# Performance work log

Measured on AMD Instinct MI355X. Metric: run time of the kernel, lower is better.

The kernel has to match this reference:

```python
import jax, jax.numpy as jnp
import numpy as np

B, S, V, K = 8, 128, 32000, 32


def setup_inputs() -> dict:
    key = jax.random.key(0)
    ks = jax.random.split(key, 8)
    return {
        "neural_logit": jax.random.normal(ks[0], (B, S, V), dtype=jnp.float32),
        "optor_vals": jax.random.randint(ks[1], (B, S, K), 0, V),
        "optor_dists": jax.random.uniform(ks[2], (B, S, K), dtype=jnp.float32) * 100.0,
        "const_vals": jax.random.randint(ks[3], (B, S, K), 0, V),
        "const_dists": jax.random.uniform(ks[4], (B, S, K), dtype=jnp.float32) * 100.0,
        "prev_words": jax.random.randint(ks[5], (B, S), 0, V),
        "optor_lamda": jnp.array([0.7], dtype=jnp.float32),
        "const_lamda": jnp.array([0.7], dtype=jnp.float32),
        "optor_temp": jnp.array([10.0], dtype=jnp.float32),
        "const_temp": jnp.array([10.0], dtype=jnp.float32),
    }


def _knn_prob(vals, dists, temp, vocab):
    # kernel-density: softmax over negative distances, scatter-add into vocab ids
    b, s, k = vals.shape
    w = jax.nn.softmax(-dists / temp, axis=-1)            # [B,S,K]
    rows = jnp.arange(b * s)[:, None]                     # [BS,1]
    p = jnp.zeros((b * s, vocab), w.dtype)
    p = p.at[rows, vals.reshape(b * s, k)].add(w.reshape(b * s, k))
    return p.reshape(b, s, vocab)


def reference(neural_logit, optor_vals, optor_dists, const_vals, const_dists,
              prev_words, optor_lamda, const_lamda, optor_temp, const_temp):
    nmt_prob = jax.nn.softmax(neural_logit, axis=-1)      # [B,S,V]

    optor_knn = _knn_prob(optor_vals, optor_dists, optor_temp[0], V)
    optor_combined = optor_lamda[0] * optor_knn + (1.0 - optor_lamda[0]) * nmt_prob

    const_knn = _knn_prob(const_vals, const_dists, const_temp[0], V)
    const_combined = const_lamda[0] * const_knn + (1.0 - const_lamda[0]) * nmt_prob

    pw = prev_words                                        # [B,S]
    optor_mask = (pw <= 88) | ((pw >= 91) & (pw <= 291))
    const_mask = (pw == 89) | (pw == 90) | (pw >= 292)

    combined = (optor_combined * optor_mask[:, :, None].astype(nmt_prob.dtype)
                + const_combined * const_mask[:, :, None].astype(nmt_prob.dtype))
    return combined
```

## Files before the change

### kernel.cpp

```cpp
#include <hip/hip_runtime.h>
#include <math.h>

constexpr int Bc = 8, Sc = 128, Vc = 32000, Kc = 32;
constexpr int ROWS = Bc * Sc;
constexpr int V4 = Vc / 4;
constexpr int NTA = 256;
constexpr int NTB = 256;
constexpr int CHUNKS = 4;
constexpr int CHUNK_F4 = V4 / CHUNKS;

typedef float v4f __attribute__((ext_vector_type(4)));

__global__ __launch_bounds__(NTA) void knn_reduce_kernel(
    const float* __restrict__ logit,
    const int*   __restrict__ prev_words,
    const float* __restrict__ optor_lamda,
    const float* __restrict__ const_lamda,
    float* __restrict__ ws)
{
    const int row = blockIdx.x;
    const int t   = threadIdx.x;
    const v4f* __restrict__ x = (const v4f*)(logit + (size_t)row * Vc);

    float m = -INFINITY, s = 0.f;
#pragma unroll 4
    for (int i = t; i < V4; i += NTA) {
        const v4f v = x[i];
        const float m4 = fmaxf(fmaxf(v.x, v.y), fmaxf(v.z, v.w));
        const float mn = fmaxf(m, m4);
        s = s * __expf(m - mn)
          + __expf(v.x - mn) + __expf(v.y - mn)
          + __expf(v.z - mn) + __expf(v.w - mn);
        m = mn;
    }
#pragma unroll
    for (int off = 32; off > 0; off >>= 1) {
        const float m2 = __shfl_xor(m, off);
        const float s2 = __shfl_xor(s, off);
        const float mn = fmaxf(m, m2);
        s = s * __expf(m - mn) + s2 * __expf(m2 - mn);
        m = mn;
    }
    __shared__ float rm[NTA / 64], rs[NTA / 64];
    const int wave = t >> 6;
    if ((t & 63) == 0) { rm[wave] = m; rs[wave] = s; }
    __syncthreads();
    if (t == 0) {
        float M = rm[0];
#pragma unroll
        for (int w = 1; w < NTA / 64; ++w) M = fmaxf(M, rm[w]);
        float Z = 0.f;
#pragma unroll
        for (int w = 0; w < NTA / 64; ++w) Z += rs[w] * __expf(rm[w] - M);

        const int pw = prev_words[row];
        const bool om = (pw <= 88) || (pw >= 91 && pw <= 291);
        const bool cm = (pw == 89) || (pw == 90) || (pw >= 292);
        const float cn = (1.f - optor_lamda[0]) * (om ? 1.f : 0.f)
                       + (1.f - const_lamda[0]) * (cm ? 1.f : 0.f);
        ws[2 * row]     = M;
        ws[2 * row + 1] = cn / Z;
    }
}

__global__ __launch_bounds__(NTB) void knn_map_kernel(
    const float* __restrict__ logit,
    const float* __restrict__ ws,
    float* __restrict__ out)
{
    const int row = blockIdx.x;
    const int t   = threadIdx.x;
    const float M  = ws[2 * row];
    const float sc = ws[2 * row + 1];
    const size_t base4 = (size_t)row * V4;
    const v4f* __restrict__ x = (const v4f*)logit + base4;
    v4f* __restrict__       o = (v4f*)out + base4;
    const int begin = blockIdx.y * CHUNK_F4;
    const int end   = begin + CHUNK_F4;
#pragma unroll 4
    for (int i = begin + t; i < end; i += NTB) {
        v4f v = x[i];
        v.x = __expf(v.x - M) * sc;
        v.y = __expf(v.y - M) * sc;
        v.z = __expf(v.z - M) * sc;
        v.w = __expf(v.w - M) * sc;
        __builtin_nontemporal_store(v, &o[i]);
    }
}

__global__ __launch_bounds__(64) void knn_scatter_kernel(
    const int*   __restrict__ optor_vals,
    const float* __restrict__ optor_dists,
    const int*   __restrict__ const_vals,
    const float* __restrict__ const_dists,
    const int*   __restrict__ prev_words,
    const float* __restrict__ optor_lamda,
    const float* __restrict__ const_lamda,
    const float* __restrict__ optor_temp,
    const float* __restrict__ const_temp,
    float* __restrict__ out)
{
    const int row = blockIdx.x;
    const int t   = threadIdx.x;
    const bool is_opt = (t < 32);
    const int k = t & 31;

    const int pw = prev_words[row];
    const bool om = (pw <= 88) || (pw >= 91 && pw <= 291);
    const bool cm = (pw == 89) || (pw == 90) || (pw >= 292);
    const float scale = is_opt ? optor_lamda[0] * (om ? 1.f : 0.f)
                               : const_lamda[0] * (cm ? 1.f : 0.f);

    const int*   vals  = is_opt ? optor_vals  : const_vals;
    const float* dists = is_opt ? optor_dists : const_dists;
    const float  temp  = is_opt ? optor_temp[0] : const_temp[0];

    const float sv = -dists[row * Kc + k] / temp;
    float mx = sv;
#pragma unroll
    for (int off = 16; off > 0; off >>= 1)
        mx = fmaxf(mx, __shfl_xor(mx, off));
    const float e = __expf(sv - mx);
    float sm = e;
#pragma unroll
    for (int off = 16; off > 0; off >>= 1)
        sm += __shfl_xor(sm, off);
    const float w = e / sm;

    if (scale != 0.f)
        atomicAdd(out + (size_t)row * Vc + vals[row * Kc + k], scale * w);
}

extern "C" void kernel_launch(void* const* d_in, const int* in_sizes, int n_in,
                              void* d_out, int out_size, void* d_ws, size_t ws_size,
                              hipStream_t stream) {
    const float* logit       = (const float*)d_in[0];
    const int*   optor_vals  = (const int*)  d_in[1];
    const float* optor_dists = (const float*)d_in[2];
    const int*   const_vals  = (const int*)  d_in[3];
    const float* const_dists = (const float*)d_in[4];
    const int*   prev_words  = (const int*)  d_in[5];
    const float* optor_lamda = (const float*)d_in[6];
    const float* const_lamda = (const float*)d_in[7];
    const float* optor_temp  = (const float*)d_in[8];
    const float* const_temp  = (const float*)d_in[9];
    float* out = (float*)d_out;
    float* ws  = (float*)d_ws;

    knn_reduce_kernel<<<ROWS, NTA, 0, stream>>>(
        logit, prev_words, optor_lamda, const_lamda, ws);

    knn_map_kernel<<<dim3(ROWS, CHUNKS), NTB, 0, stream>>>(logit, ws, out);

    knn_scatter_kernel<<<ROWS, 64, 0, stream>>>(
        optor_vals, optor_dists, const_vals, const_dists, prev_words,
        optor_lamda, const_lamda, optor_temp, const_temp, out);
}
```

Before: 271.0 us.

## Split row reduction into chunks and fuse kNN scatter into map kernel

The reduce kernel now runs a 2D grid of row×chunk blocks and writes a partial max and sum per chunk. The map kernel merges the four partials itself and applies the per-row mask and lambda scaling. It also performs the kNN softmax and atomic scatter for the vocab ids that fall in its own chunk, after a block barrier. This removes one kernel launch and raises parallelism in the reduction pass. It also changes the output store from nontemporal to a normal store, which may keep lines in cache for the atomics but could add cache pressure.

```diff
diff --git a/kernel.cpp b/kernel.cpp
--- a/kernel.cpp
+++ b/kernel.cpp
@@ -4,27 +4,26 @@
 constexpr int Bc = 8, Sc = 128, Vc = 32000, Kc = 32;
 constexpr int ROWS = Bc * Sc;
 constexpr int V4 = Vc / 4;
-constexpr int NTA = 256;
-constexpr int NTB = 256;
 constexpr int CHUNKS = 4;
 constexpr int CHUNK_F4 = V4 / CHUNKS;
+constexpr int NT = 256;
 
 typedef float v4f __attribute__((ext_vector_type(4)));
 
-__global__ __launch_bounds__(NTA) void knn_reduce_kernel(
+__global__ __launch_bounds__(NT) void knn_reduce_kernel(
     const float* __restrict__ logit,
-    const int*   __restrict__ prev_words,
-    const float* __restrict__ optor_lamda,
-    const float* __restrict__ const_lamda,
     float* __restrict__ ws)
 {
     const int row = blockIdx.x;
+    const int c   = blockIdx.y;
     const int t   = threadIdx.x;
     const v4f* __restrict__ x = (const v4f*)(logit + (size_t)row * Vc);
+    const int begin = c * CHUNK_F4;
+    const int end   = begin + CHUNK_F4;
 
     float m = -INFINITY, s = 0.f;
 #pragma unroll 4
-    for (int i = t; i < V4; i += NTA) {
+    for (int i = begin + t; i < end; i += NT) {
         const v4f v = x[i];
         const float m4 = fmaxf(fmaxf(v.x, v.y), fmaxf(v.z, v.w));
         const float mn = fmaxf(m, m4);
@@ -41,54 +40,26 @@
         s = s * __expf(m - mn) + s2 * __expf(m2 - mn);
         m = mn;
     }
-    __shared__ float rm[NTA / 64], rs[NTA / 64];
+    __shared__ float rm[NT / 64], rs[NT / 64];
     const int wave = t >> 6;
     if ((t & 63) == 0) { rm[wave] = m; rs[wave] = s; }
     __syncthreads();
     if (t == 0) {
         float M = rm[0];
 #pragma unroll
-        for (int w = 1; w < NTA / 64; ++w) M = fmaxf(M, rm[w]);
-        float Z = 0.f;
+        for (int w = 1; w < NT / 64; ++w) M = fmaxf(M, rm[w]);
+        float S = 0.f;
 #pragma unroll
-        for (int w = 0; w < NTA / 64; ++w) Z += rs[w] * __expf(rm[w] - M);
-
-        const int pw = prev_words[row];
-        const bool om = (pw <= 88) || (pw >= 91 && pw <= 291);
-        const bool cm = (pw == 89) || (pw == 90) || (pw >= 292);
-        const float cn = (1.f - optor_lamda[0]) * (om ? 1.f : 0.f)
-                       + (1.f - const_lamda[0]) * (cm ? 1.f : 0.f);
-        ws[2 * row]     = M;
-        ws[2 * row + 1] = cn / Z;
+        for (int w = 0; w < NT / 64; ++w) S += rs[w] * __expf(rm[w] - M);
+        const int slot = (row * CHUNKS + c) * 2;
+        ws[slot]     = M;
+        ws[slot + 1] = S;
     }
 }
 
-__global__ __launch_bounds__(NTB) void knn_map_kernel(
+__global__ __launch_bounds__(NT) void knn_map_kernel(
     const float* __restrict__ logit,
     const float* __restrict__ ws,
-    float* __restrict__ out)
-{
-    const int row = blockIdx.x;
-    const int t   = threadIdx.x;
-    const float M  = ws[2 * row];
-    const float sc = ws[2 * row + 1];
-    const size_t base4 = (size_t)row * V4;
-    const v4f* __restrict__ x = (const v4f*)logit + base4;
-    v4f* __restrict__       o = (v4f*)out + base4;
-    const int begin = blockIdx.y * CHUNK_F4;
-    const int end   = begin + CHUNK_F4;
-#pragma unroll 4
-    for (int i = begin + t; i < end; i += NTB) {
-        v4f v = x[i];
-        v.x = __expf(v.x - M) * sc;
-        v.y = __expf(v.y - M) * sc;
-        v.z = __expf(v.z - M) * sc;
-        v.w = __expf(v.w - M) * sc;
-        __builtin_nontemporal_store(v, &o[i]);
-    }
-}
-
-__global__ __launch_bounds__(64) void knn_scatter_kernel(
     const int*   __restrict__ optor_vals,
     const float* __restrict__ optor_dists,
     const int*   __restrict__ const_vals,
@@ -101,34 +72,64 @@
     float* __restrict__ out)
 {
     const int row = blockIdx.x;
+    const int c   = blockIdx.y;
     const int t   = threadIdx.x;
-    const bool is_opt = (t < 32);
-    const int k = t & 31;
+
+    const float* p = ws + row * CHUNKS * 2;
+    float M = fmaxf(fmaxf(p[0], p[2]), fmaxf(p[4], p[6]));
+    float Z = p[1] * __expf(p[0] - M) + p[3] * __expf(p[2] - M)
+            + p[5] * __expf(p[4] - M) + p[7] * __expf(p[6] - M);
 
     const int pw = prev_words[row];
     const bool om = (pw <= 88) || (pw >= 91 && pw <= 291);
     const bool cm = (pw == 89) || (pw == 90) || (pw >= 292);
-    const float scale = is_opt ? optor_lamda[0] * (om ? 1.f : 0.f)
-                               : const_lamda[0] * (cm ? 1.f : 0.f);
+    const float omf = om ? 1.f : 0.f;
+    const float cmf = cm ? 1.f : 0.f;
+    const float ol = optor_lamda[0];
+    const float cl = const_lamda[0];
+    const float sc = ((1.f - ol) * omf + (1.f - cl) * cmf) / Z;
 
-    const int*   vals  = is_opt ? optor_vals  : const_vals;
-    const float* dists = is_opt ? optor_dists : const_dists;
-    const float  temp  = is_opt ? optor_temp[0] : const_temp[0];
+    const size_t base4 = (size_t)row * V4;
+    const v4f* __restrict__ x = (const v4f*)logit + base4;
+    v4f* __restrict__       o = (v4f*)out + base4;
+    const int begin = c * CHUNK_F4;
+    const int end   = begin + CHUNK_F4;
+#pragma unroll 4
+    for (int i = begin + t; i < end; i += NT) {
+        v4f v = x[i];
+        v.x = __expf(v.x - M) * sc;
+        v.y = __expf(v.y - M) * sc;
+        v.z = __expf(v.z - M) * sc;
+        v.w = __expf(v.w - M) * sc;
+        o[i] = v;
+    }
 
-    const float sv = -dists[row * Kc + k] / temp;
-    float mx = sv;
+    __syncthreads();
+
+    if (t < 64) {
+        const bool is_opt = (t < 32);
+        const int k = t & 31;
+        const float scale = is_opt ? ol * omf : cl * cmf;
+        const int*   vals  = is_opt ? optor_vals  : const_vals;
+        const float* dists = is_opt ? optor_dists : const_dists;
+        const float  temp  = is_opt ? optor_temp[0] : const_temp[0];
+
+        const float sv = -dists[row * Kc + k] / temp;
+        float mx = sv;
 #pragma unroll
-    for (int off = 16; off > 0; off >>= 1)
-        mx = fmaxf(mx, __shfl_xor(mx, off));
-    const float e = __expf(sv - mx);
-    float sm = e;
+        for (int off = 16; off > 0; off >>= 1)
+            mx = fmaxf(mx, __shfl_xor(mx, off));
+        const float e = __expf(sv - mx);
+        float sm = e;
 #pragma unroll
-    for (int off = 16; off > 0; off >>= 1)
-        sm += __shfl_xor(sm, off);
-    const float w = e / sm;
+        for (int off = 16; off > 0; off >>= 1)
+            sm += __shfl_xor(sm, off);
+        const float w = e / sm;
 
-    if (scale != 0.f)
-        atomicAdd(out + (size_t)row * Vc + vals[row * Kc + k], scale * w);
+        const int val = vals[row * Kc + k];
+        if (scale != 0.f && val >= begin * 4 && val < end * 4)
+            atomicAdd(out + (size_t)row * Vc + val, scale * w);
+    }
 }
 
 extern "C" void kernel_launch(void* const* d_in, const int* in_sizes, int n_in,
@@ -147,12 +148,9 @@
     float* out = (float*)d_out;
     float* ws  = (float*)d_ws;
 
-    knn_reduce_kernel<<<ROWS, NTA, 0, stream>>>(
-        logit, prev_words, optor_lamda, const_lamda, ws);
+    knn_reduce_kernel<<<dim3(ROWS, CHUNKS), NT, 0, stream>>>(logit, ws);
 
-    knn_map_kernel<<<dim3(ROWS, CHUNKS), NTB, 0, stream>>>(logit, ws, out);
-
-    knn_scatter_kernel<<<ROWS, 64, 0, stream>>>(
-        optor_vals, optor_dists, const_vals, const_dists, prev_words,
-        optor_lamda, const_lamda, optor_temp, const_temp, out);
+    knn_map_kernel<<<dim3(ROWS, CHUNKS), NT, 0, stream>>>(
+        logit, ws, optor_vals, optor_dists, const_vals, const_dists,
+        prev_words, optor_lamda, const_lamda, optor_temp, const_temp, out);
 }
```

Measured after the change: 272.3 us. About the same (+0.5%).
